# Optimization experiments

Measured on AMD Instinct MI355X. Metric: run time of the kernel, lower is better.

Reference implementation:

```python
import jax, jax.numpy as jnp
import numpy as np

N = 50000      # nodes
E = 800000     # edges (before self loops)
D_IN = 128
D_H = 128
NEG_SLOPE = 0.2  # GATv2Conv default


def setup_inputs() -> dict:
    key = jax.random.key(0)
    ks = jax.random.split(key, 32)
    it = iter(range(32))
    def nk():
        return ks[next(it)]
    def p(shape, scale=0.05):
        return jax.random.normal(nk(), shape, jnp.float32) * scale
    inp = {
        "x": jax.random.normal(nk(), (N, D_IN), jnp.float32),
        "edge_index": jax.random.randint(nk(), (2, E), 0, N, jnp.int32),
        "edge_attr": jax.random.uniform(nk(), (E, 1), jnp.float32),
    }
    dims = [(D_IN, D_H), (D_H, D_H), (D_H, D_H)]
    for i, (di, do) in enumerate(dims, 1):
        inp[f"Wl{i}"] = p((di, do))   # lin_l (source)
        inp[f"Wr{i}"] = p((di, do))   # lin_r (target)
        inp[f"We{i}"] = p((1, do))    # lin_edge (edge_dim=1, no bias)
        inp[f"att{i}"] = p((do,))     # attention vector a
        inp[f"b{i}"] = jnp.zeros((do,), jnp.float32)
    inp["Wlin"] = p((D_H, 1))
    inp["blin"] = jnp.zeros((1,), jnp.float32)
    return inp


def _gatv2(x, src, dst, ew, Wl, Wr, We, att, b):
    # GATv2Conv, heads=1: e = a^T LeakyReLU(Wl x_j + Wr x_i + We ea),
    # alpha = segment_softmax(e over dst), out_i = sum_j alpha * Wl x_j + b
    xl = x @ Wl                       # [N, C] source transform
    xr = x @ Wr                       # [N, C] target transform
    ee = ew @ We                      # [E', C] edge embedding
    s = jax.nn.leaky_relu(xl[src] + xr[dst] + ee, NEG_SLOPE)  # [E', C]
    logits = s @ att                  # [E']
    m = jax.ops.segment_max(logits, dst, num_segments=N)
    e = jnp.exp(logits - m[dst])
    denom = jax.ops.segment_sum(e, dst, num_segments=N)
    alpha = e / denom[dst]            # [E'] segment softmax
    out = jax.ops.segment_sum(alpha[:, None] * xl[src], dst, num_segments=N)
    return out + b


def reference(x, edge_index, edge_attr,
              Wl1, Wr1, We1, att1, b1,
              Wl2, Wr2, We2, att2, b2,
              Wl3, Wr3, We3, att3, b3,
              Wlin, blin):
    # edge_weights = 1/edge_attr, zeros -> 1/1e-4
    zero = edge_attr == 0
    ew = jnp.where(zero, 10000.0, 1.0 / jnp.where(zero, 1.0, edge_attr))
    src, dst = edge_index[0], edge_index[1]
    # add self loops with fill_value=0 edge attr
    loop = jnp.arange(N, dtype=src.dtype)
    src = jnp.concatenate([src, loop])
    dst = jnp.concatenate([dst, loop])
    ew = jnp.concatenate([ew, jnp.zeros((N, 1), ew.dtype)])

    h = jax.nn.relu(_gatv2(x, src, dst, ew, Wl1, Wr1, We1, att1, b1))
    h = jax.nn.relu(_gatv2(h, src, dst, ew, Wl2, Wr2, We2, att2, b2))
    h = _gatv2(h, src, dst, ew, Wl3, Wr3, We3, att3, b3)
    return (h @ Wlin + blin).squeeze(-1)   # [N]
```

## Files before the change

### kernel.cpp

```cpp
#include <hip/hip_runtime.h>
#include <math.h>

#define NN 50000
#define EE 800000
#define EP 850000
#define DD 128
#define NEG_SLOPE 0.2f

typedef float f4 __attribute__((ext_vector_type(4)));

__global__ void k_hist(const int* __restrict__ ei, int* __restrict__ counts) {
    int e = blockIdx.x * blockDim.x + threadIdx.x;
    if (e >= EP) return;
    int dst = (e < EE) ? ei[EE + e] : (e - EE);
    atomicAdd(&counts[dst], 1);
}

__global__ void k_scan1(const int* __restrict__ counts, int* __restrict__ row_ptr,
                        int* __restrict__ blockSums) {
    __shared__ int wsum[16];
    int t = threadIdx.x;
    int lane = t & 63;
    int wave = t >> 6;
    int g = blockIdx.x * 1024 + t;
    int v = (g < NN) ? counts[g] : 0;

    int s = v;
#pragma unroll
    for (int o = 1; o < 64; o <<= 1) {
        int u = __shfl_up(s, o, 64);
        if (lane >= o) s += u;
    }
    if (lane == 63) wsum[wave] = s;
    __syncthreads();
    if (wave == 0) {
        int ws = (lane < 16) ? wsum[lane] : 0;
#pragma unroll
        for (int o = 1; o < 16; o <<= 1) {
            int u = __shfl_up(ws, o, 64);
            if (lane >= o) ws += u;
        }
        if (lane < 16) wsum[lane] = ws;
    }
    __syncthreads();
    int base = (wave > 0) ? wsum[wave - 1] : 0;
    int incl = base + s;
    if (g < NN) row_ptr[g] = incl - v;
    if (t == 1023) blockSums[blockIdx.x] = incl;
}

__global__ void k_scan2(const int* __restrict__ blockSums, int* __restrict__ blockOffs,
                        int nb, int* __restrict__ row_ptr) {
    if (threadIdx.x == 0 && blockIdx.x == 0) {
        int run = 0;
        for (int i = 0; i < nb; ++i) { blockOffs[i] = run; run += blockSums[i]; }
        row_ptr[NN] = run;
    }
}

__global__ void k_scan3(int* __restrict__ row_ptr, const int* __restrict__ blockOffs) {
    int g = blockIdx.x * 1024 + threadIdx.x;
    if (g < NN) row_ptr[g] += blockOffs[blockIdx.x];
}

__global__ void k_scatter(const int* __restrict__ ei, const float* __restrict__ eattr,
                          const int* __restrict__ row_ptr, int* __restrict__ fill,
                          int* __restrict__ src_sorted, float* __restrict__ ew_sorted) {
    int e = blockIdx.x * blockDim.x + threadIdx.x;
    if (e >= EP) return;
    int s, d; float w;
    if (e < EE) {
        s = ei[e]; d = ei[EE + e];
        float a = eattr[e];
        w = (a == 0.0f) ? 10000.0f : (1.0f / a);
    } else {
        s = d = e - EE;
        w = 0.0f;
    }
    int pos = row_ptr[d] + atomicAdd(&fill[d], 1);
    src_sorted[pos] = s;
    ew_sorted[pos] = w;
}

#define GD_BM 64
#define KC 8
__global__ __launch_bounds__(256, 2) void k_gemm_dual(const float* __restrict__ X,
        const float* __restrict__ Wl, const float* __restrict__ Wr,
        float* __restrict__ xl, float* __restrict__ xr, int nrows) {
    __shared__ f4 xs[GD_BM][32];
    __shared__ f4 wls[2][KC][32];
    __shared__ f4 wrs[2][KC][32];
    int t = threadIdx.x;
    int rowbase = blockIdx.x * GD_BM;

#pragma unroll
    for (int i = 0; i < 8; ++i) {
        int idx = t + i * 256;
        int r = idx >> 5, kk = idx & 31;
        int gr = rowbase + r;
        f4 v = {0.f, 0.f, 0.f, 0.f};
        if (gr < nrows) v = *(const f4*)&X[gr * DD + kk * 4];
        xs[r][kk] = v;
    }
    int wk = t >> 5, wc = t & 31;
    wls[0][wk][wc] = *(const f4*)&Wl[wk * DD + wc * 4];
    wrs[0][wk][wc] = *(const f4*)&Wr[wk * DD + wc * 4];
    __syncthreads();

    int c0 = t & 31;
    int r0 = (t >> 5) * 8;
    f4 accL[8], accR[8];
#pragma unroll
    for (int i = 0; i < 8; ++i) { accL[i] = (f4){0,0,0,0}; accR[i] = (f4){0,0,0,0}; }

    int buf = 0;
    for (int ch = 0; ch < 16; ++ch) {
        f4 pl, pr;
        if (ch < 15) {
            int kg = (ch + 1) * KC + wk;
            pl = *(const f4*)&Wl[kg * DD + wc * 4];
            pr = *(const f4*)&Wr[kg * DD + wc * 4];
        }
#pragma unroll
        for (int k4 = 0; k4 < KC / 4; ++k4) {
            f4 a[8];
#pragma unroll
            for (int i = 0; i < 8; ++i) a[i] = xs[r0 + i][ch * 2 + k4];
#pragma unroll
            for (int j = 0; j < 4; ++j) {
                f4 wl = wls[buf][k4 * 4 + j][c0];
                f4 wr = wrs[buf][k4 * 4 + j][c0];
#pragma unroll
                for (int i = 0; i < 8; ++i) {
                    float av = a[i][j];
                    accL[i] += av * wl;
                    accR[i] += av * wr;
                }
            }
        }
        if (ch < 15) {
            wls[buf ^ 1][wk][wc] = pl;
            wrs[buf ^ 1][wk][wc] = pr;
            __syncthreads();
        }
        buf ^= 1;
    }

#pragma unroll
    for (int i = 0; i < 8; ++i) {
        int row = rowbase + r0 + i;
        if (row < nrows) {
            *(f4*)&xl[row * DD + c0 * 4] = accL[i];
            *(f4*)&xr[row * DD + c0 * 4] = accR[i];
        }
    }
}

__device__ inline f4 lrelu4(f4 v) {
    f4 r;
    r.x = v.x > 0.f ? v.x : NEG_SLOPE * v.x;
    r.y = v.y > 0.f ? v.y : NEG_SLOPE * v.y;
    r.z = v.z > 0.f ? v.z : NEG_SLOPE * v.z;
    r.w = v.w > 0.f ? v.w : NEG_SLOPE * v.w;
    return r;
}

template<bool DO_RELU, bool FUSE_FINAL>
__global__ __launch_bounds__(256) void k_agg_t(const float* __restrict__ xl,
        const float* __restrict__ xr, const int* __restrict__ row_ptr,
        const int* __restrict__ src_sorted, const float* __restrict__ ew_sorted,
        const float* __restrict__ We, const float* __restrict__ att,
        const float* __restrict__ bias, float* __restrict__ out,
        const float* __restrict__ Wlin, const float* __restrict__ blin,
        float* __restrict__ outS) {
    int wid = (blockIdx.x * blockDim.x + threadIdx.x) >> 6;
    int lane = threadIdx.x & 63;
    if (wid >= NN) return;
    int quarter = lane >> 4;
    int c = (lane & 15) * 8;

    const f4 xrv0 = *(const f4*)&xr[wid * DD + c];
    const f4 xrv1 = *(const f4*)&xr[wid * DD + c + 4];
    const f4 att0 = *(const f4*)&att[c];
    const f4 att1 = *(const f4*)&att[c + 4];
    const f4 We0  = *(const f4*)&We[c];
    const f4 We1  = *(const f4*)&We[c + 4];

    int beg = row_ptr[wid];
    int end = row_ptr[wid + 1];
    int niter = (end - beg + 3) >> 2;

    float m = -1e30f;
    float d = 0.0f;
    f4 acc0 = {0,0,0,0}, acc1 = {0,0,0,0};

    int e0 = beg + quarter;
    bool val_cur = (e0 < end);
    int ee0 = val_cur ? e0 : (end - 1);
    float w_cur = ew_sorted[ee0];
    int s_cur = src_sorted[ee0];
    f4 x0c = *(const f4*)&xl[s_cur * DD + c];
    f4 x1c = *(const f4*)&xl[s_cur * DD + c + 4];

    for (int i = 0; i < niter; ++i) {
        f4 x0n = {0,0,0,0}, x1n = {0,0,0,0};
        float w_nxt = 0.f; bool val_nxt = false;
        if (i + 1 < niter) {
            int e = beg + 4 * (i + 1) + quarter;
            val_nxt = (e < end);
            int ee = val_nxt ? e : (end - 1);
            w_nxt = ew_sorted[ee];
            int sn = src_sorted[ee];
            x0n = *(const f4*)&xl[sn * DD + c];
            x1n = *(const f4*)&xl[sn * DD + c + 4];
        }

        f4 t0 = lrelu4(x0c + xrv0 + w_cur * We0);
        f4 t1 = lrelu4(x1c + xrv1 + w_cur * We1);
        float p = t0.x * att0.x + t0.y * att0.y + t0.z * att0.z + t0.w * att0.w
                + t1.x * att1.x + t1.y * att1.y + t1.z * att1.z + t1.w * att1.w;
#pragma unroll
        for (int o = 8; o >= 1; o >>= 1) p += __shfl_xor(p, o, 64);

        float logit = val_cur ? p : -1e30f;
        float nm = fmaxf(m, logit);
        float sc = __expf(m - nm);
        float pe = __expf(logit - nm);
        d = d * sc + pe;
        acc0 = acc0 * sc + pe * x0c;
        acc1 = acc1 * sc + pe * x1c;
        m = nm;

        x0c = x0n; x1c = x1n; w_cur = w_nxt; val_cur = val_nxt;
    }

#pragma unroll
    for (int o = 16; o <= 32; o <<= 1) {
        float mo = __shfl_xor(m, o, 64);
        float dn = __shfl_xor(d, o, 64);
        f4 a0o, a1o;
        a0o.x = __shfl_xor(acc0.x, o, 64); a0o.y = __shfl_xor(acc0.y, o, 64);
        a0o.z = __shfl_xor(acc0.z, o, 64); a0o.w = __shfl_xor(acc0.w, o, 64);
        a1o.x = __shfl_xor(acc1.x, o, 64); a1o.y = __shfl_xor(acc1.y, o, 64);
        a1o.z = __shfl_xor(acc1.z, o, 64); a1o.w = __shfl_xor(acc1.w, o, 64);
        float M  = fmaxf(m, mo);
        float sA = __expf(m - M);
        float sB = __expf(mo - M);
        d = d * sA + dn * sB;
        acc0 = acc0 * sA + a0o * sB;
        acc1 = acc1 * sA + a1o * sB;
        m = M;
    }

    if (quarter == 0) {
        float inv = 1.0f / d;
        f4 bv0 = *(const f4*)&bias[c];
        f4 bv1 = *(const f4*)&bias[c + 4];
        f4 o0 = acc0 * inv + bv0;
        f4 o1 = acc1 * inv + bv1;
        if (DO_RELU) {
            o0.x = fmaxf(o0.x, 0.f); o0.y = fmaxf(o0.y, 0.f);
            o0.z = fmaxf(o0.z, 0.f); o0.w = fmaxf(o0.w, 0.f);
            o1.x = fmaxf(o1.x, 0.f); o1.y = fmaxf(o1.y, 0.f);
            o1.z = fmaxf(o1.z, 0.f); o1.w = fmaxf(o1.w, 0.f);
        }
        if (FUSE_FINAL) {
            f4 wl0 = *(const f4*)&Wlin[c];
            f4 wl1 = *(const f4*)&Wlin[c + 4];
            float p = o0.x * wl0.x + o0.y * wl0.y + o0.z * wl0.z + o0.w * wl0.w
                    + o1.x * wl1.x + o1.y * wl1.y + o1.z * wl1.z + o1.w * wl1.w;
#pragma unroll
            for (int o = 8; o >= 1; o >>= 1) p += __shfl_xor(p, o, 64);
            if (lane == 0) outS[wid] = p + blin[0];
        } else {
            *(f4*)&out[wid * DD + c] = o0;
            *(f4*)&out[wid * DD + c + 4] = o1;
        }
    }
}

static inline size_t align256(size_t x) { return (x + 255) & ~(size_t)255; }

extern "C" void kernel_launch(void* const* d_in, const int* in_sizes, int n_in,
                              void* d_out, int out_size, void* d_ws, size_t ws_size,
                              hipStream_t stream) {
    const float* x     = (const float*)d_in[0];
    const int*   ei    = (const int*)d_in[1];
    const float* eattr = (const float*)d_in[2];
    const float* Wl[3]  = {(const float*)d_in[3],  (const float*)d_in[8],  (const float*)d_in[13]};
    const float* Wr[3]  = {(const float*)d_in[4],  (const float*)d_in[9],  (const float*)d_in[14]};
    const float* We[3]  = {(const float*)d_in[5],  (const float*)d_in[10], (const float*)d_in[15]};
    const float* att[3] = {(const float*)d_in[6],  (const float*)d_in[11], (const float*)d_in[16]};
    const float* bb[3]  = {(const float*)d_in[7],  (const float*)d_in[12], (const float*)d_in[17]};
    const float* Wlin = (const float*)d_in[18];
    const float* blin = (const float*)d_in[19];

    char* p = (char*)d_ws;
    int* counts = (int*)p;          p += align256((size_t)NN * 4);
    int* fill   = (int*)p;          p += align256((size_t)NN * 4);
    int* row_ptr= (int*)p;          p += align256((size_t)(NN + 1) * 4);
    int* blockSums = (int*)p;       p += align256(64 * 4);
    int* blockOffs = (int*)p;       p += align256(64 * 4);
    int* src_sorted = (int*)p;      p += align256((size_t)EP * 4);
    float* ew_sorted = (float*)p;   p += align256((size_t)EP * 4);
    float* xl = (float*)p;          p += align256((size_t)NN * DD * 4);
    float* xr = (float*)p;          p += align256((size_t)NN * DD * 4);
    float* hA = (float*)p;          p += align256((size_t)NN * DD * 4);
    float* hB = (float*)p;          p += align256((size_t)NN * DD * 4);

    hipMemsetAsync(counts, 0, align256((size_t)NN * 4) + align256((size_t)NN * 4), stream);

    const int nb_scan = (NN + 1023) / 1024;
    k_hist<<<(EP + 255) / 256, 256, 0, stream>>>(ei, counts);
    k_scan1<<<nb_scan, 1024, 0, stream>>>(counts, row_ptr, blockSums);
    k_scan2<<<1, 64, 0, stream>>>(blockSums, blockOffs, nb_scan, row_ptr);
    k_scan3<<<nb_scan, 1024, 0, stream>>>(row_ptr, blockOffs);
    k_scatter<<<(EP + 255) / 256, 256, 0, stream>>>(ei, eattr, row_ptr, fill, src_sorted, ew_sorted);

    const int gemm_grid = (NN + GD_BM - 1) / GD_BM;
    const int agg_grid  = (NN + 3) / 4;

    k_gemm_dual<<<gemm_grid, 256, 0, stream>>>(x, Wl[0], Wr[0], xl, xr, NN);
    k_agg_t<true, false><<<agg_grid, 256, 0, stream>>>(xl, xr, row_ptr, src_sorted, ew_sorted,
                                        We[0], att[0], bb[0], hA, nullptr, nullptr, nullptr);
    k_gemm_dual<<<gemm_grid, 256, 0, stream>>>(hA, Wl[1], Wr[1], xl, xr, NN);
    k_agg_t<true, false><<<agg_grid, 256, 0, stream>>>(xl, xr, row_ptr, src_sorted, ew_sorted,
                                        We[1], att[1], bb[1], hB, nullptr, nullptr, nullptr);
    k_gemm_dual<<<gemm_grid, 256, 0, stream>>>(hB, Wl[2], Wr[2], xl, xr, NN);
    k_agg_t<false, true><<<agg_grid, 256, 0, stream>>>(xl, xr, row_ptr, src_sorted, ew_sorted,
                                        We[2], att[2], bb[2], nullptr, Wlin, blin, (float*)d_out);
}
```

Before: 555.7 us.

## Replace FP32 SIMT dual GEMM with split-bf16 MFMA GEMM

The scalar FP32 dual GEMM (x@Wl, x@Wr) is replaced by a matrix-core kernel using bf16 MFMA 16x16x32. Each operand is split into high and low bf16 parts and three products are summed to approximate FP32 accuracy. Weights are pre-packed once per call into the MFMA fragment layout. The input tile is converted to bf16 hi/lo in swizzled shared memory to avoid bank conflicts. This trades three times the MFMA work and a small numerical precision loss for much higher matrix throughput than FP32 FMAs.

```diff
diff --git a/kernel.cpp b/kernel.cpp
--- a/kernel.cpp
+++ b/kernel.cpp
@@ -7,7 +7,19 @@
 #define DD 128
 #define NEG_SLOPE 0.2f
 
-typedef float f4 __attribute__((ext_vector_type(4)));
+typedef float f4  __attribute__((ext_vector_type(4)));
+typedef float f32x4 __attribute__((ext_vector_type(4)));
+typedef short bf16x8 __attribute__((ext_vector_type(8)));
+typedef short s4 __attribute__((ext_vector_type(4)));
+
+static __device__ inline short f2bf(float f) {
+    unsigned u = __float_as_uint(f);
+    unsigned r = (u + 0x7FFFu + ((u >> 16) & 1u)) >> 16;
+    return (short)r;
+}
+static __device__ inline float bf2f(short s) {
+    return __uint_as_float(((unsigned)(unsigned short)s) << 16);
+}
 
 __global__ void k_hist(const int* __restrict__ ei, int* __restrict__ counts) {
     int e = blockIdx.x * blockDim.x + threadIdx.x;
@@ -82,76 +94,110 @@
     ew_sorted[pos] = w;
 }
 
-#define GD_BM 64
-#define KC 8
-__global__ __launch_bounds__(256, 2) void k_gemm_dual(const float* __restrict__ X,
-        const float* __restrict__ Wl, const float* __restrict__ Wr,
+__global__ void k_wpack(const float* __restrict__ W0, const float* __restrict__ W1,
+                        const float* __restrict__ W2, const float* __restrict__ W3,
+                        const float* __restrict__ W4, const float* __restrict__ W5,
+                        short* __restrict__ dst) {
+    int mat = blockIdx.x >> 6;
+    int e = ((blockIdx.x & 63) << 8) + threadIdx.x;
+    const float* W = (mat == 0) ? W0 : (mat == 1) ? W1 : (mat == 2) ? W2
+                   : (mat == 3) ? W3 : (mat == 4) ? W4 : W5;
+    int k = e >> 7, c = e & 127;
+    float w = W[e];
+    short hb = f2bf(w);
+    short lb = f2bf(w - bf2f(hb));
+    int ks = k >> 5, kk = k & 31, g = kk >> 3, j = kk & 7, ct = c >> 4, cl = c & 15;
+    int off = ((ks * 8 + ct) * 64 + (g * 16 + cl)) * 8 + j;
+    int base = (mat >> 1) * 65536 + (mat & 1) * 32768;
+    dst[base + off] = hb;
+    dst[base + 16384 + off] = lb;
+}
+
+#define GB_ROWS 128
+__global__ __launch_bounds__(256, 2) void k_gemm_mfma(const float* __restrict__ X,
+        const short* __restrict__ Wpk,
         float* __restrict__ xl, float* __restrict__ xr, int nrows) {
-    __shared__ f4 xs[GD_BM][32];
-    __shared__ f4 wls[2][KC][32];
-    __shared__ f4 wrs[2][KC][32];
+    __shared__ short xh[128 * 128];
+    __shared__ short xlo[128 * 128];
     int t = threadIdx.x;
-    int rowbase = blockIdx.x * GD_BM;
-
-#pragma unroll
-    for (int i = 0; i < 8; ++i) {
+    int rowbase = blockIdx.x * GB_ROWS;
+
+#pragma unroll
+    for (int i = 0; i < 16; ++i) {
         int idx = t + i * 256;
-        int r = idx >> 5, kk = idx & 31;
+        int r = idx >> 5;
+        int k4 = idx & 31;
+        f4 v = {0.f, 0.f, 0.f, 0.f};
         int gr = rowbase + r;
-        f4 v = {0.f, 0.f, 0.f, 0.f};
-        if (gr < nrows) v = *(const f4*)&X[gr * DD + kk * 4];
-        xs[r][kk] = v;
-    }
-    int wk = t >> 5, wc = t & 31;
-    wls[0][wk][wc] = *(const f4*)&Wl[wk * DD + wc * 4];
-    wrs[0][wk][wc] = *(const f4*)&Wr[wk * DD + wc * 4];
+        if (gr < nrows) v = *(const f4*)&X[gr * DD + k4 * 4];
+        s4 h, l;
+#pragma unroll
+        for (int j = 0; j < 4; ++j) {
+            short hb = f2bf(v[j]);
+            h[j] = hb;
+            l[j] = f2bf(v[j] - bf2f(hb));
+        }
+        int si = r * 128 + (((k4 >> 1) ^ (r & 7)) << 3) + (k4 & 1) * 4;
+        *(s4*)&xh[si] = h;
+        *(s4*)&xlo[si] = l;
+    }
     __syncthreads();
 
-    int c0 = t & 31;
-    int r0 = (t >> 5) * 8;
-    f4 accL[8], accR[8];
-#pragma unroll
-    for (int i = 0; i < 8; ++i) { accL[i] = (f4){0,0,0,0}; accR[i] = (f4){0,0,0,0}; }
-
-    int buf = 0;
-    for (int ch = 0; ch < 16; ++ch) {
-        f4 pl, pr;
-        if (ch < 15) {
-            int kg = (ch + 1) * KC + wk;
-            pl = *(const f4*)&Wl[kg * DD + wc * 4];
-            pr = *(const f4*)&Wr[kg * DD + wc * 4];
-        }
-#pragma unroll
-        for (int k4 = 0; k4 < KC / 4; ++k4) {
-            f4 a[8];
-#pragma unroll
-            for (int i = 0; i < 8; ++i) a[i] = xs[r0 + i][ch * 2 + k4];
-#pragma unroll
-            for (int j = 0; j < 4; ++j) {
-                f4 wl = wls[buf][k4 * 4 + j][c0];
-                f4 wr = wrs[buf][k4 * 4 + j][c0];
-#pragma unroll
-                for (int i = 0; i < 8; ++i) {
-                    float av = a[i][j];
-                    accL[i] += av * wl;
-                    accR[i] += av * wr;
+    int wave = t >> 6, lane = t & 63;
+    int wr = wave >> 1, wc = wave & 1;
+
+    f32x4 acc[4][4][2];
+#pragma unroll
+    for (int rt = 0; rt < 4; ++rt)
+#pragma unroll
+        for (int ct = 0; ct < 4; ++ct) {
+            acc[rt][ct][0] = (f32x4){0.f, 0.f, 0.f, 0.f};
+            acc[rt][ct][1] = (f32x4){0.f, 0.f, 0.f, 0.f};
+        }
+
+    for (int ks = 0; ks < 4; ++ks) {
+        bf16x8 Ah[4], Al[4];
+#pragma unroll
+        for (int rt = 0; rt < 4; ++rt) {
+            int row = wr * 64 + rt * 16 + (lane & 15);
+            int slot = ks * 4 + (lane >> 4);
+            int si = row * 128 + ((slot ^ (row & 7)) << 3);
+            Ah[rt] = *(const bf16x8*)&xh[si];
+            Al[rt] = *(const bf16x8*)&xlo[si];
+        }
+#pragma unroll
+        for (int ct = 0; ct < 4; ++ct) {
+            int ctg = wc * 4 + ct;
+            int fb = ((ks * 8 + ctg) * 64 + lane) * 8;
+            bf16x8 Blh = *(const bf16x8*)&Wpk[fb];
+            bf16x8 Bll = *(const bf16x8*)&Wpk[16384 + fb];
+            bf16x8 Brh = *(const bf16x8*)&Wpk[32768 + fb];
+            bf16x8 Brl = *(const bf16x8*)&Wpk[49152 + fb];
+#pragma unroll
+            for (int rt = 0; rt < 4; ++rt) {
+                acc[rt][ct][0] = __builtin_amdgcn_mfma_f32_16x16x32_bf16(Ah[rt], Blh, acc[rt][ct][0], 0, 0, 0);
+                acc[rt][ct][0] = __builtin_amdgcn_mfma_f32_16x16x32_bf16(Ah[rt], Bll, acc[rt][ct][0], 0, 0, 0);
+                acc[rt][ct][0] = __builtin_amdgcn_mfma_f32_16x16x32_bf16(Al[rt], Blh, acc[rt][ct][0], 0, 0, 0);
+                acc[rt][ct][1] = __builtin_amdgcn_mfma_f32_16x16x32_bf16(Ah[rt], Brh, acc[rt][ct][1], 0, 0, 0);
+                acc[rt][ct][1] = __builtin_amdgcn_mfma_f32_16x16x32_bf16(Ah[rt], Brl, acc[rt][ct][1], 0, 0, 0);
+                acc[rt][ct][1] = __builtin_amdgcn_mfma_f32_16x16x32_bf16(Al[rt], Brh, acc[rt][ct][1], 0, 0, 0);
+            }
+        }
+    }
+
+#pragma unroll
+    for (int rt = 0; rt < 4; ++rt) {
+#pragma unroll
+        for (int reg = 0; reg < 4; ++reg) {
+            int row = rowbase + wr * 64 + rt * 16 + (lane >> 4) * 4 + reg;
+            if (row < nrows) {
+#pragma unroll
+                for (int ct = 0; ct < 4; ++ct) {
+                    int col = wc * 64 + ct * 16 + (lane & 15);
+                    xl[row * DD + col] = acc[rt][ct][0][reg];
+                    xr[row * DD + col] = acc[rt][ct][1][reg];
                 }
             }
-        }
-        if (ch < 15) {
-            wls[buf ^ 1][wk][wc] = pl;
-            wrs[buf ^ 1][wk][wc] = pr;
-            __syncthreads();
-        }
-        buf ^= 1;
-    }
-
-#pragma unroll
-    for (int i = 0; i < 8; ++i) {
-        int row = rowbase + r0 + i;
-        if (row < nrows) {
-            *(f4*)&xl[row * DD + c0 * 4] = accL[i];
-            *(f4*)&xr[row * DD + c0 * 4] = accR[i];
         }
     }
 }
@@ -307,6 +353,7 @@
     float* xr = (float*)p;          p += align256((size_t)NN * DD * 4);
     float* hA = (float*)p;          p += align256((size_t)NN * DD * 4);
     float* hB = (float*)p;          p += align256((size_t)NN * DD * 4);
+    short* wpk = (short*)p;         p += align256((size_t)3 * 65536 * 2);
 
     hipMemsetAsync(counts, 0, align256((size_t)NN * 4) + align256((size_t)NN * 4), stream);
 
@@ -317,16 +364,18 @@
     k_scan3<<<nb_scan, 1024, 0, stream>>>(row_ptr, blockOffs);
     k_scatter<<<(EP + 255) / 256, 256, 0, stream>>>(ei, eattr, row_ptr, fill, src_sorted, ew_sorted);
 
-    const int gemm_grid = (NN + GD_BM - 1) / GD_BM;
+    k_wpack<<<6 * 64, 256, 0, stream>>>(Wl[0], Wr[0], Wl[1], Wr[1], Wl[2], Wr[2], wpk);
+
+    const int gemm_grid = (NN + GB_ROWS - 1) / GB_ROWS;
     const int agg_grid  = (NN + 3) / 4;
 
-    k_gemm_dual<<<gemm_grid, 256, 0, stream>>>(x, Wl[0], Wr[0], xl, xr, NN);
+    k_gemm_mfma<<<gemm_grid, 256, 0, stream>>>(x, wpk + 0 * 65536, xl, xr, NN);
     k_agg_t<true, false><<<agg_grid, 256, 0, stream>>>(xl, xr, row_ptr, src_sorted, ew_sorted,
                                         We[0], att[0], bb[0], hA, nullptr, nullptr, nullptr);
-    k_gemm_dual<<<gemm_grid, 256, 0, stream>>>(hA, Wl[1], Wr[1], xl, xr, NN);
+    k_gemm_mfma<<<gemm_grid, 256, 0, stream>>>(hA, wpk + 1 * 65536, xl, xr, NN);
     k_agg_t<true, false><<<agg_grid, 256, 0, stream>>>(xl, xr, row_ptr, src_sorted, ew_sorted,
                                         We[1], att[1], bb[1], hB, nullptr, nullptr, nullptr);
-    k_gemm_dual<<<gemm_grid, 256, 0, stream>>>(hB, Wl[2], Wr[2], xl, xr, NN);
+    k_gemm_mfma<<<gemm_grid, 256, 0, stream>>>(hB, wpk + 2 * 65536, xl, xr, NN);
     k_agg_t<false, true><<<agg_grid, 256, 0, stream>>>(xl, xr, row_ptr, src_sorted, ew_sorted,
                                         We[2], att[2], bb[2], nullptr, Wlin, blin, (float*)d_out);
 }
```

Result: faster. 479.6 us (-13.7%).
